# Optimization experiments

Measured on AMD Instinct MI355X. Metric: run time of the kernel, lower is better.

## Reference

```python
import jax, jax.numpy as jnp
import numpy as np

H, DK, DIM, DFF, DEPTH = 8, 64, 512, 2048, 8
B, LS, LT, VOCAB = 16, 128, 128, 32000


def setup_inputs() -> dict:
    key = jax.random.key(0)
    ks = jax.random.split(key, 20)
    w = lambda k, s: jax.random.normal(k, s, jnp.float32) * 0.02
    N_enc, N_dec = B * LS, B * LT
    base_s = np.arange(B) * LS
    base_t = np.arange(B) * LT
    i = np.arange(LS)
    j = np.arange(LT)
    # encoder self-attn: full bipartite within each sentence
    ee_src = (base_s[:, None, None] + i[None, :, None] + 0 * i[None, None, :]).reshape(-1)
    ee_dst = (base_s[:, None, None] + 0 * i[None, :, None] + i[None, None, :]).reshape(-1)
    # decoder self-attn: causal (key pos <= query pos)
    ii, jj = np.meshgrid(j, j, indexing='ij')  # ii = dst(query) pos, jj = src(key) pos
    m = jj <= ii
    dd_src = (base_t[:, None] + jj[m][None, :]).reshape(-1)
    dd_dst = (base_t[:, None] + ii[m][None, :]).reshape(-1)
    # cross-attn: enc node -> dec node, full within sentence
    ed_src = (base_s[:, None, None] + i[None, :, None] + 0 * j[None, None, :]).reshape(-1)
    ed_dst = (base_t[:, None, None] + 0 * i[None, :, None] + j[None, None, :]).reshape(-1)
    return {
        'emb_src': w(ks[0], (VOCAB, DIM)), 'emb_tgt': w(ks[1], (VOCAB, DIM)),
        'pos_emb': w(ks[2], (LS, DIM)), 'time_emb': w(ks[3], (DEPTH, DIM)),
        'Wqkv_e': w(ks[4], (DIM, 3 * DIM)), 'Wo_e': w(ks[5], (DIM, DIM)),
        'W1_e': w(ks[6], (DIM, DFF)), 'W2_e': w(ks[7], (DFF, DIM)),
        'Wqkv_d': w(ks[8], (DIM, 3 * DIM)), 'Wo_d': w(ks[9], (DIM, DIM)),
        'W1_d': w(ks[10], (DIM, DFF)), 'W2_d': w(ks[11], (DFF, DIM)),
        'Wq_x': w(ks[12], (DIM, DIM)), 'Wkv_x': w(ks[13], (DIM, 2 * DIM)),
        'Wo_x': w(ks[14], (DIM, DIM)), 'Wgen': w(ks[15], (DIM, VOCAB)),
        'src_tokens': jax.random.randint(ks[16], (N_enc,), 0, VOCAB, jnp.int32),
        'tgt_tokens': jax.random.randint(ks[17], (N_dec,), 0, VOCAB, jnp.int32),
        'src_pos': jnp.tile(jnp.arange(LS, dtype=jnp.int32), B),
        'tgt_pos': jnp.tile(jnp.arange(LT, dtype=jnp.int32), B),
        'ee_src': jnp.asarray(ee_src, jnp.int32), 'ee_dst': jnp.asarray(ee_dst, jnp.int32),
        'dd_src': jnp.asarray(dd_src, jnp.int32), 'dd_dst': jnp.asarray(dd_dst, jnp.int32),
        'ed_src': jnp.asarray(ed_src, jnp.int32), 'ed_dst': jnp.asarray(ed_dst, jnp.int32),
    }


def _ln(x):
    m = x.mean(-1, keepdims=True)
    v = ((x - m) ** 2).mean(-1, keepdims=True)
    return (x - m) * jax.lax.rsqrt(v + 1e-5)


def _attn(q, k, v, src, dst, n_dst):
    # q: [Nq,H,DK] (dst side), k/v: [Nk,H,DK] (src side); edge lists [E]
    # src_dot_dst -> scaled_exp -> scatter-sum (src_mul_edge + sum, copy_edge + sum), then wv/z
    s = jnp.exp(jnp.einsum('ehd,ehd->eh', k[src], q[dst]) / np.float32(np.sqrt(DK)))  # [E,H]
    wv = jax.ops.segment_sum(s[:, :, None] * v[src], dst, num_segments=n_dst)  # [Nq,H,DK]
    z = jax.ops.segment_sum(s, dst, num_segments=n_dst)  # [Nq,H]
    return (wv / (z[:, :, None] + 1e-9)).reshape(n_dst, DIM)


def reference(emb_src, emb_tgt, pos_emb, time_emb, Wqkv_e, Wo_e, W1_e, W2_e,
              Wqkv_d, Wo_d, W1_d, W2_d, Wq_x, Wkv_x, Wo_x, Wgen,
              src_tokens, tgt_tokens, src_pos, tgt_pos,
              ee_src, ee_dst, dd_src, dd_dst, ed_src, ed_dst):
    Ne, Nd = src_tokens.shape[0], tgt_tokens.shape[0]
    x_e = emb_src[src_tokens] + pos_emb[src_pos]
    x_d = emb_tgt[tgt_tokens] + pos_emb[tgt_pos]
    # encoder: MAX_DEPTH shared-weight iterations with time+pos enc re-added each step
    for t in range(DEPTH):
        xp = x_e + pos_emb[src_pos] + time_emb[t]
        q, k, v = jnp.split(xp @ Wqkv_e, 3, axis=-1)
        o = _attn(q.reshape(Ne, H, DK), k.reshape(Ne, H, DK), v.reshape(Ne, H, DK), ee_src, ee_dst, Ne)
        x_e = _ln(x_e + o @ Wo_e)
        x_e = _ln(x_e + jax.nn.relu(x_e @ W1_e) @ W2_e)
    # decoder: self-attn (causal dd) then cross-attn (ed) each iteration
    for t in range(DEPTH):
        xp = x_d + pos_emb[tgt_pos] + time_emb[t]
        q, k, v = jnp.split(xp @ Wqkv_d, 3, axis=-1)
        o = _attn(q.reshape(Nd, H, DK), k.reshape(Nd, H, DK), v.reshape(Nd, H, DK), dd_src, dd_dst, Nd)
        x_d = _ln(x_d + o @ Wo_d)
        qx = ((x_d + pos_emb[tgt_pos] + time_emb[t]) @ Wq_x).reshape(Nd, H, DK)
        kx, vx = jnp.split(x_e @ Wkv_x, 2, axis=-1)
        o = _attn(qx, kx.reshape(Ne, H, DK), vx.reshape(Ne, H, DK), ed_src, ed_dst, Nd)
        x_d = _ln(x_d + o @ Wo_x)
        x_d = _ln(x_d + jax.nn.relu(x_d @ W1_d) @ W2_d)
    return jax.nn.log_softmax(x_d @ Wgen, axis=-1)  # generator over dec nodes
```

## Files before the change

### kernel.cpp

```cpp
#include <hip/hip_runtime.h>
#include <hip/hip_bf16.h>
#include <math.h>

#define H 8
#define DK 64
#define DIM 512
#define DFF 2048
#define DEPTH 8
#define VOCAB 32000
#define NTOK 2048

typedef float f32x4 __attribute__((ext_vector_type(4)));
typedef short bf16x8 __attribute__((ext_vector_type(8)));

static __device__ __forceinline__ unsigned short f2bf(float f) {
    unsigned u = __float_as_uint(f);
    return (unsigned short)((u + 0x7FFFu + ((u >> 16) & 1u)) >> 16);
}

#define GLL(src, dst) __builtin_amdgcn_global_load_lds( \
    (const __attribute__((address_space(1))) unsigned int*)(src), \
    (__attribute__((address_space(3))) unsigned int*)(dst), 16, 0, 0)

static __device__ __forceinline__ void load_ln_stats(
// ... 79 lines not shown

    for (int k0 = 0; k0 < K; k0 += 64) {
        if (k0) __syncthreads();
#pragma unroll
        for (int it = 0; it < 4; it++) {
            int q = (wid * 4 + it) * 64 + lane;
            int row = q >> 3;
            int cs = (q & 7) ^ (row & 7);
            GLL(Bt + (size_t)(n0 + row) * K + k0 + cs * 8, &Bsm[(wid * 4 + it) * 512]);
        }
#pragma unroll
        for (int it = 0; it < 4; it++) {
            int q = (wid * 4 + it) * 64 + lane;
            int row = q >> 3;
            int cs = q & 7;
            const float* s = Tf + (size_t)(m0 + row) * K + k0 + cs * 8;
            float4 u0 = *(const float4*)s, u1 = *(const float4*)(s + 4);
            float m = Lm[row], iv = Li[row];
            unsigned short c8[8];
            c8[0] = f2bf((u0.x - m) * iv); c8[1] = f2bf((u0.y - m) * iv);
            c8[2] = f2bf((u0.z - m) * iv); c8[3] = f2bf((u0.w - m) * iv);
            c8[4] = f2bf((u1.x - m) * iv); c8[5] = f2bf((u1.y - m) * iv);
            c8[6] = f2bf((u1.z - m) * iv); c8[7] = f2bf((u1.w - m) * iv);
            *(bf16x8*)&Asm[row * 64 + ((cs ^ (row & 7)) * 8)] = *(bf16x8*)c8;
        }
        __syncthreads();
#pragma unroll
        for (int kk = 0; kk < 2; kk++) {
            bf16x8 af[4], bfr[4];
#pragma unroll
            for (int i = 0; i < 4; i++) {
                int rowA = wm + i * 16 + (lane & 15);
                int ca = (kk * 4 + (lane >> 4)) ^ (rowA & 7);
                af[i] = *(const bf16x8*)&Asm[rowA * 64 + ca * 8];
                int rowB = wn + i * 16 + (lane & 15);
                int cb = (kk * 4 + (lane >> 4)) ^ (rowB & 7);
                bfr[i] = *(const bf16x8*)&Bsm[rowB * 64 + cb * 8];
            }
#pragma unroll
            for (int i = 0; i < 4; i++)
#pragma unroll
                for (int j = 0; j < 4; j++)
                    acc[i][j] = __builtin_amdgcn_mfma_f32_16x16x32_bf16(af[i], bfr[j], acc[i][j], 0, 0, 0);
        }
    }
#pragma unroll
    for (int i = 0; i < 4; i++)
#pragma unroll
        for (int j = 0; j < 4; j++)
#pragma unroll
            for (int r = 0; r < 4; r++) {
                int row = m0 + wm + i * 16 + (lane >> 4) * 4 + r;
                int col = n0 + wn + j * 16 + (lane & 15);
                size_t idx = (size_t)row * N + col;
                float v = acc[i][j][r];
                if (EPI == 1) Cb[idx] = f2bf(fmaxf(v, 0.f));
                if (EPI == 3) Cb[idx] = f2bf(v);
            }
}

__global__ __launch_bounds__(256) void gemm_bb(
    const unsigned short* __restrict__ A,
    const unsigned short* __restrict__ Bt,
    const float* __restrict__ Tin,
    const float* __restrict__ statsIn,
    float* __restrict__ Tout,
    float* __restrict__ statsOut,
    int M, int K)
{
    __shared__ __align__(16) unsigned short Asm[64 * 64];
    __shared__ __align__(16) unsigned short Bsm[64 * 64];
    __shared__ float Lm[64], Li[64];
    __shared__ float sredS[4][64], sredQ[4][64];
    const int tid = threadIdx.x;
    const int lane = tid & 63, wid = tid >> 6;
    const int nb = blockIdx.x;
    const int m0 = blockIdx.y * 64, n0 = nb * 64;
    const int wm = (wid >> 1) * 32, wn = (wid & 1) * 32;

    load_ln_stats(statsIn, m0, 64, Lm, Li, tid, 256);
    __syncthreads();

    f32x4 acc[2][2];
#pragma unroll
    for (int i = 0; i < 2; i++)
#pragma unroll
        for (int j = 0; j < 2; j++) acc[i][j] = (f32x4){0.f, 0.f, 0.f, 0.f};

    for (int k0 = 0; k0 < K; k0 += 64) {
        if (k0) __syncthreads();
#pragma unroll
        for (int it = 0; it < 2; it++) {
            int q = it * 256 + tid;
            int row = q >> 3;
            int cs = (q & 7) ^ (row & 7);
            GLL(A + (size_t)(m0 + row) * K + k0 + cs * 8, &Asm[(it * 256 + wid * 64) * 8]);
            GLL(Bt + (size_t)(n0 + row) * K + k0 + cs * 8, &Bsm[(it * 256 + wid * 64) * 8]);
        }
        __syncthreads();
#pragma unroll
        for (int kd = 0; kd < 2; kd++) {
            bf16x8 af[2], bfr[2];
#pragma unroll
            for (int i = 0; i < 2; i++) {
                int rowA = wm + i * 16 + (lane & 15);
                int ca = (kd * 4 + (lane >> 4)) ^ (rowA & 7);
                af[i] = *(const bf16x8*)&Asm[rowA * 64 + ca * 8];
                int rowB = wn + i * 16 + (lane & 15);
                int cb = (kd * 4 + (lane >> 4)) ^ (rowB & 7);
                bfr[i] = *(const bf16x8*)&Bsm[rowB * 64 + cb * 8];
            }
#pragma unroll
            for (int i = 0; i < 2; i++)
#pragma unroll
                for (int j = 0; j < 2; j++)
                    acc[i][j] = __builtin_amdgcn_mfma_f32_16x16x32_bf16(af[i], bfr[j], acc[i][j], 0, 0, 0);
        }
    }
#pragma unroll
    for (int i = 0; i < 2; i++) {
#pragma unroll
        for (int r = 0; r < 4; r++) {
            int rl = wm + i * 16 + (lane >> 4) * 4 + r;
            int row = m0 + rl;
            float s = 0.f, q = 0.f;
#pragma unroll
            for (int j = 0; j < 2; j++) {
                int col = n0 + wn + j * 16 + (lane & 15);
                size_t idx = (size_t)row * DIM + col;
                float rv = (Tin[idx] - Lm[rl]) * Li[rl];
                float v = acc[i][j][r] + rv;
                Tout[idx] = v;
                s += v; q += v * v;
            }
            s += __shfl_xor(s, 1); s += __shfl_xor(s, 2);
            s += __shfl_xor(s, 4); s += __shfl_xor(s, 8);
            q += __shfl_xor(q, 1); q += __shfl_xor(q, 2);
            q += __shfl_xor(q, 4); q += __shfl_xor(q, 8);
            if ((lane & 15) == 0) { sredS[wid][rl] = s; sredQ[wid][rl] = q; }
        }
    }
    __syncthreads();
    if (tid < 64) {
        int row = tid;
        int w0 = (row >= 32) ? 2 : 0;
        float s = sredS[w0][row] + sredS[w0 + 1][row];
        float q = sredQ[w0][row] + sredQ[w0 + 1][row];
        statsOut[(size_t)(m0 + row) * 16 + nb * 2] = s;
        statsOut[(size_t)(m0 + row) * 16 + nb * 2 + 1] = q;
    }
}

template<int CAUSAL>
static __device__ __forceinline__ void attn_core16(
    const unsigned short* Qs, const unsigned short* Ks, const unsigned short* Vt,
    unsigned short* Psw, int wq, int lane, int tok0, int h,
    unsigned short* __restrict__ O)
{
    bf16x8 qa[2];
#pragma unroll
    for (int kd = 0; kd < 2; kd++) {
        int qr = wq + (lane & 15);
        int ch = (kd * 4 + (lane >> 4)) ^ (qr & 7);
        qa[kd] = *(const bf16x8*)&Qs[qr * 64 + ch * 8];
    }
    const int kcmax = CAUSAL ? ((wq >> 5) + 1) : 4;
    const int jmax = CAUSAL ? (kcmax * 2) : 8;

    float zr[4] = {0.f, 0.f, 0.f, 0.f};
    f32x4 oacc[4];
#pragma unroll
    for (int dt = 0; dt < 4; dt++) oacc[dt] = (f32x4){0.f, 0.f, 0.f, 0.f};

    for (int kb = 0; kb < 2; kb++) {
        int j0 = kb * 4;
        if (j0 >= jmax) break;
        int jn = jmax - j0; if (jn > 4) jn = 4;
        f32x4 sacc[4];
#pragma unroll
        for (int j = 0; j < 4; j++) sacc[j] = (f32x4){0.f, 0.f, 0.f, 0.f};
#pragma unroll 2
        for (int kd = 0; kd < 2; kd++) {
            for (int jj = 0; jj < jn; jj++) {
                int kr = (j0 + jj) * 16 + (lane & 15);
                int ch = (kd * 4 + (lane >> 4)) ^ (kr & 7);
                bf16x8 kf = *(const bf16x8*)&Ks[kr * 64 + ch * 8];
                sacc[jj] = __builtin_amdgcn_mfma_f32_16x16x32_bf16(qa[kd], kf, sacc[jj], 0, 0, 0);
            }
        }
        int qbase = wq + (lane >> 4) * 4;
        for (int jj = 0; jj < jn; jj++) {
            int kcol = (j0 + jj) * 16 + (lane & 15);
#pragma unroll
            for (int rr = 0; rr < 4; rr++) {
                float p = __expf(sacc[jj][rr] * 0.125f);
                if (CAUSAL && kcol > qbase + rr) p = 0.f;
                zr[rr] += p;
                int prow = (lane >> 4) * 4 + rr;
                int ch = ((jj * 2 + ((lane & 15) >> 3)) ^ (prow & 7));
                Psw[prow * 64 + ch * 8 + (lane & 7)] = f2bf(p);
            }
        }
        int kcn = kcmax - kb * 2; if (kcn > 2) kcn = 2;
        for (int kcl = 0; kcl < kcn; kcl++) {
            bf16x8 pa;
            {
                int prow = lane & 15;
                int ch = (kcl * 4 + (lane >> 4)) ^ (prow & 7);
                pa = *(const bf16x8*)&Psw[prow * 64 + ch * 8];
            }
            int kcg = kb * 2 + kcl;
#pragma unroll
            for (int dt = 0; dt < 4; dt++) {
                int d = dt * 16 + (lane & 15);
                bf16x8 vf = *(const bf16x8*)&Vt[d * 132 + (kcg * 4 + (lane >> 4)) * 8];
                oacc[dt] = __builtin_amdgcn_mfma_f32_16x16x32_bf16(pa, vf, oacc[dt], 0, 0, 0);
            }
        }
    }
#pragma unroll
    for (int rr = 0; rr < 4; rr++) {
        float z = zr[rr];
        z += __shfl_xor(z, 1); z += __shfl_xor(z, 2);
        z += __shfl_xor(z, 4); z += __shfl_xor(z, 8);
        zr[rr] = 1.f / (z + 1e-9f);
    }
#pragma unroll
    for (int dt = 0; dt < 4; dt++)
#pragma unroll
        for (int rr = 0; rr < 4; rr++) {
            int qrow = tok0 + wq + (lane >> 4) * 4 + rr;
            O[(size_t)qrow * DIM + h * 64 + dt * 16 + (lane & 15)] =
                f2bf(oacc[dt][rr] * zr[rr]);
        }
}

template<int CAUSAL>
__global__ __launch_bounds__(512) void fused_attn(
    const float* __restrict__ Tf,
    const float* __restrict__ stats,
    const float* __restrict__ pos,
    const float* __restrict__ trow,
    const unsigned short* __restrict__ WqkvT,
    unsigned short* __restrict__ O)
{
    __shared__ __align__(16) unsigned short smem[33024];
    __shared__ float LmA[128], LiA[128];
    unsigned short* Asm = smem;
    unsigned short* Bsm = smem + 8192;
    unsigned short* Qs  = smem;
    unsigned short* Ks  = smem + 8192;
    unsigned short* Vt  = smem + 16384;
    const int tid = threadIdx.x;
    const int lane = tid & 63, wid = tid >> 6;
    unsigned short* Psw = smem + 24832 + wid * 1024;
    const int b = blockIdx.x >> 3, h = blockIdx.x & 7;
    const int tok0 = b * 128;
    const int wq = wid * 16;

    load_ln_stats(stats, tok0, 128, LmA, LiA, tid, 512);
    __syncthreads();

    f32x4 acc[12];
#pragma unroll
    for (int c = 0; c < 12; c++) acc[c] = (f32x4){0.f, 0.f, 0.f, 0.f};

    for (int k0 = 0; k0 < 512; k0 += 64) {
        if (k0) __syncthreads();
#pragma unroll
        for (int it = 0; it < 3; it++) {
            int q = it * 512 + wid * 64 + lane;
            int r = q >> 3;
            int cs = (q & 7) ^ (r & 7);
            int srow = (r < 64) ? (h * 64 + r)
                     : (r < 128) ? (512 + h * 64 + (r - 64))
                                 : (1024 + h * 64 + (r - 128));
            GLL(WqkvT + (size_t)srow * 512 + k0 + cs * 8, &Bsm[(it * 512 + wid * 64) * 8]);
        }
#pragma unroll
        for (int it = 0; it < 2; it++) {
            int q = it * 512 + tid;
            int row = q >> 3;
            int cs = q & 7;
            const float* s = Tf + (size_t)(tok0 + row) * 512 + k0 + cs * 8;
            const float* pp = pos + (size_t)row * 512 + k0 + cs * 8;
            const float* tt = trow + k0 + cs * 8;
            float4 u0 = *(const float4*)s, u1 = *(const float4*)(s + 4);
            float4 p0 = *(const float4*)pp, p1 = *(const float4*)(pp + 4);
            float4 t0 = *(const float4*)tt, t1 = *(const float4*)(tt + 4);
            float m = LmA[row], iv = LiA[row];
            unsigned short c8[8];
            c8[0] = f2bf((u0.x - m) * iv + p0.x + t0.x);
            c8[1] = f2bf((u0.y - m) * iv + p0.y + t0.y);
            c8[2] = f2bf((u0.z - m) * iv + p0.z + t0.z);
            c8[3] = f2bf((u0.w - m) * iv + p0.w + t0.w);
            c8[4] = f2bf((u1.x - m) * iv + p1.x + t1.x);
            c8[5] = f2bf((u1.y - m) * iv + p1.y + t1.y);
            c8[6] = f2bf((u1.z - m) * iv + p1.z + t1.z);
            c8[7] = f2bf((u1.w - m) * iv + p1.w + t1.w);
            *(bf16x8*)&Asm[row * 64 + ((cs ^ (row & 7)) * 8)] = *(bf16x8*)c8;
        }
        __syncthreads();
#pragma unroll
        for (int kk = 0; kk < 2; kk++) {
            int rowA = wq + (lane & 15);
            int ca = (kk * 4 + (lane >> 4)) ^ (rowA & 7);
            bf16x8 af = *(const bf16x8*)&Asm[rowA * 64 + ca * 8];
#pragma unroll
            for (int c = 0; c < 12; c++) {
                int rowB = c * 16 + (lane & 15);
                int cb = (kk * 4 + (lane >> 4)) ^ (rowB & 7);
                bf16x8 bfr = *(const bf16x8*)&Bsm[rowB * 64 + cb * 8];
                acc[c] = __builtin_amdgcn_mfma_f32_16x16x32_bf16(af, bfr, acc[c], 0, 0, 0);
            }
        }
    }
    __syncthreads();
#pragma unroll
    for (int c = 0; c < 12; c++)
#pragma unroll
        for (int r = 0; r < 4; r++) {
            int token = wq + (lane >> 4) * 4 + r;
            int col = (c & 3) * 16 + (lane & 15);
            unsigned short v = f2bf(acc[c][r]);
            if (c < 4)      Qs[token * 64 + (((col >> 3) ^ (token & 7)) * 8) + (col & 7)] = v;
            else if (c < 8) Ks[token * 64 + (((col >> 3) ^ (token & 7)) * 8) + (col & 7)] = v;
            else            Vt[col * 132 + token] = v;
        }
    __syncthreads();
    attn_core16<CAUSAL>(Qs, Ks, Vt, Psw, wq, lane, tok0, h, O);
}

__global__ __launch_bounds__(512) void fused_xattn(
    const float* __restrict__ Tf,
    const float* __restrict__ stats,
    const float* __restrict__ pos,
    const float* __restrict__ trow,
    const unsigned short* __restrict__ WqT,
    const unsigned short* __restrict__ kvx,
    unsigned short* __restrict__ O)
{
    __shared__ __align__(16) unsigned short smem[33024];
    __shared__ float LmA[128], LiA[128];
    unsigned short* Asm = smem;
    unsigned short* Bsm = smem + 8192;
    unsigned short* Qs  = smem;
    unsigned short* Ks  = smem + 8192;
    unsigned short* Vt  = smem + 16384;
    const int tid = threadIdx.x;
    const int lane = tid & 63, wid = tid >> 6;
    unsigned short* Psw = smem + 24832 + wid * 1024;
    const int b = blockIdx.x >> 3, h = blockIdx.x & 7;
    const int tok0 = b * 128;
    const int wq = wid * 16;

    load_ln_stats(stats, tok0, 128, LmA, LiA, tid, 512);
    __syncthreads();

    f32x4 acc[4];
#pragma unroll
    for (int c = 0; c < 4; c++) acc[c] = (f32x4){0.f, 0.f, 0.f, 0.f};

    for (int k0 = 0; k0 < 512; k0 += 64) {
        if (k0) __syncthreads();
        {
            int q = wid * 64 + lane;
            int r = q >> 3;
            int cs = (q & 7) ^ (r & 7);
            GLL(WqT + (size_t)(h * 64 + r) * 512 + k0 + cs * 8, &Bsm[(wid * 64) * 8]);
        }
#pragma unroll
        for (int it = 0; it < 2; it++) {
            int q = it * 512 + tid;
            int row = q >> 3;
            int cs = q & 7;
            const float* s = Tf + (size_t)(tok0 + row) * 512 + k0 + cs * 8;
            const float* pp = pos + (size_t)row * 512 + k0 + cs * 8;
            const float* tt = trow + k0 + cs * 8;
            float4 u0 = *(const float4*)s, u1 = *(const float4*)(s + 4);
            float4 p0 = *(const float4*)pp, p1 = *(const float4*)(pp + 4);
            float4 t0 = *(const float4*)tt, t1 = *(const float4*)(tt + 4);
            float m = LmA[row], iv = LiA[row];
            unsigned short c8[8];
            c8[0] = f2bf((u0.x - m) * iv + p0.x + t0.x);
            c8[1] = f2bf((u0.y - m) * iv + p0.y + t0.y);
            c8[2] = f2bf((u0.z - m) * iv + p0.z + t0.z);
            c8[3] = f2bf((u0.w - m) * iv + p0.w + t0.w);
            c8[4] = f2bf((u1.x - m) * iv + p1.x + t1.x);
            c8[5] = f2bf((u1.y - m) * iv + p1.y + t1.y);
            c8[6] = f2bf((u1.z - m) * iv + p1.z + t1.z);
            c8[7] = f2bf((u1.w - m) * iv + p1.w + t1.w);
            *(bf16x8*)&Asm[row * 64 + ((cs ^ (row & 7)) * 8)] = *(bf16x8*)c8;
        }
        __syncthreads();
#pragma unroll
        for (int kk = 0; kk < 2; kk++) {
            int rowA = wq + (lane & 15);
            int ca = (kk * 4 + (lane >> 4)) ^ (rowA & 7);
            bf16x8 af = *(const bf16x8*)&Asm[rowA * 64 + ca * 8];
#pragma unroll
            for (int c = 0; c < 4; c++) {
                int rowB = c * 16 + (lane & 15);
                int cb = (kk * 4 + (lane >> 4)) ^ (rowB & 7);
                bf16x8 bfr = *(const bf16x8*)&Bsm[rowB * 64 + cb * 8];
                acc[c] = __builtin_amdgcn_mfma_f32_16x16x32_bf16(af, bfr, acc[c], 0, 0, 0);
            }
        }
    }
    __syncthreads();
#pragma unroll
    for (int c = 0; c < 4; c++)
#pragma unroll
        for (int r = 0; r < 4; r++) {
            int token = wq + (lane >> 4) * 4 + r;
            int col = c * 16 + (lane & 15);
            Qs[token * 64 + (((col >> 3) ^ (token & 7)) * 8) + (col & 7)] = f2bf(acc[c][r]);
        }
    {
        int r = tid >> 2, c0 = (tid & 3) * 2;
        const unsigned short* Kg = kvx + (size_t)(tok0 + r) * 1024 + h * 64;
        const unsigned short* Vg = Kg + 512;
#pragma unroll
        for (int c = c0; c < c0 + 2; c++) {
            bf16x8 kv = *(const bf16x8*)&Kg[c * 8];
            *(bf16x8*)&Ks[r * 64 + ((c ^ (r & 7)) * 8)] = kv;
            bf16x8 vv = *(const bf16x8*)&Vg[c * 8];
#pragma unroll
            for (int j = 0; j < 8; j++)
                Vt[(c * 8 + j) * 132 + r] = (unsigned short)vv[j];
        }
    }
    __syncthreads();
    attn_core16<0>(Qs, Ks, Vt, Psw, wq, lane, tok0, h, O);
}

__global__ __launch_bounds__(64) void ln_fin(const float* __restrict__ T,
                                             const float* __restrict__ stats,
                                             unsigned short* __restrict__ outb) {
    const int row = blockIdx.x, lane = threadIdx.x;
    const float* st = stats + (size_t)row * 16;
    float sum = 0.f, sq = 0.f;
#pragma unroll
    for (int b = 0; b < 8; b++) { sum += st[b * 2]; sq += st[b * 2 + 1]; }
    float m = sum * (1.f / 512.f);
    float v = sq * (1.f / 512.f) - m * m;
    float inv = 1.f / sqrtf(v + 1e-5f);
    const float* p = T + (size_t)row * DIM;
    unsigned short* qb = outb + (size_t)row * DIM;
#pragma unroll
    for (int i = 0; i < 8; i++)
        qb[lane + i * 64] = f2bf((p[lane + i * 64] - m) * inv);
}

__global__ __launch_bounds__(512) void gemm_gen(
    const unsigned short* __restrict__ Ab,
    const unsigned short* __restrict__ Bt,
    float* __restrict__ Out,
    float* __restrict__ pm,
    float* __restrict__ psum)
{
    __shared__ __align__(16) unsigned short Asm[256 * 64];
    __shared__ __align__(16) unsigned short Bsm[128 * 64];
    __shared__ float pml[8][64];
    __shared__ float psl[8][64];
    const int tid = threadIdx.x;
    const int lane = tid & 63, wid = tid >> 6;
    const int m0 = blockIdx.x * 256, n0 = blockIdx.y * 128;
    const int wm = (wid >> 1) * 64, wn = (wid & 1) * 64;

    f32x4 acc[4][4];
#pragma unroll
    for (int i = 0; i < 4; i++)
#pragma unroll
        for (int j = 0; j < 4; j++) acc[i][j] = (f32x4){0.f, 0.f, 0.f, 0.f};

    for (int k0 = 0; k0 < 512; k0 += 64) {
        if (k0) __syncthreads();
#pragma unroll
        for (int it = 0; it < 2; it++) {
            int q = it * 512 + tid;
            int row = q >> 3;
            int cs = (q & 7) ^ (row & 7);
            GLL(Bt + (size_t)(n0 + row) * 512 + k0 + cs * 8, &Bsm[(it * 512 + wid * 64) * 8]);
        }
#pragma unroll
        for (int it = 0; it < 4; it++) {
            int q = it * 512 + tid;
            int row = q >> 3;
            int cs = (q & 7) ^ (row & 7);
            GLL(Ab + (size_t)(m0 + row) * 512 + k0 + cs * 8, &Asm[(it * 512 + wid * 64) * 8]);
        }
        __syncthreads();
#pragma unroll
        for (int kk = 0; kk < 2; kk++) {
            bf16x8 af[4], bfr[4];
#pragma unroll
            for (int i = 0; i < 4; i++) {
                int rowA = wm + i * 16 + (lane & 15);
                int ca = (kk * 4 + (lane >> 4)) ^ (rowA & 7);
                af[i] = *(const bf16x8*)&Asm[rowA * 64 + ca * 8];
                int rowB = wn + i * 16 + (lane & 15);
                int cb = (kk * 4 + (lane >> 4)) ^ (rowB & 7);
                bfr[i] = *(const bf16x8*)&Bsm[rowB * 64 + cb * 8];
            }
#pragma unroll
            for (int i = 0; i < 4; i++)
#pragma unroll
                for (int j = 0; j < 4; j++)
                    acc[i][j] = __builtin_amdgcn_mfma_f32_16x16x32_bf16(af[i], bfr[j], acc[i][j], 0, 0, 0);
        }
    }
#pragma unroll
    for (int i = 0; i < 4; i++) {
#pragma unroll
        for (int r = 0; r < 4; r++) {
            float mx = fmaxf(fmaxf(acc[i][0][r], acc[i][1][r]),
                             fmaxf(acc[i][2][r], acc[i][3][r]));
            mx = fmaxf(mx, __shfl_xor(mx, 1));
            mx = fmaxf(mx, __shfl_xor(mx, 2));
            mx = fmaxf(mx, __shfl_xor(mx, 4));
            mx = fmaxf(mx, __shfl_xor(mx, 8));
            float s = __expf(acc[i][0][r] - mx) + __expf(acc[i][1][r] - mx) +
                      __expf(acc[i][2][r] - mx) + __expf(acc[i][3][r] - mx);
            s += __shfl_xor(s, 1); s += __shfl_xor(s, 2);
            s += __shfl_xor(s, 4); s += __shfl_xor(s, 8);
            if ((lane & 15) == 0) {
                int li = i * 16 + (lane >> 4) * 4 + r;
                pml[wid][li] = mx;
                psl[wid][li] = s;
            }
        }
    }
    __syncthreads();
    if (tid < 256) {
        int g = tid >> 6, lr = tid & 63;
        int wa = g * 2, wb = g * 2 + 1;
        float ma = pml[wa][lr], mb = pml[wb][lr];
        float m = fmaxf(ma, mb);
        float s = psl[wa][lr] * __expf(ma - m) + psl[wb][lr] * __expf(mb - m);
        pm[(size_t)(m0 + g * 64 + lr) * 256 + blockIdx.y] = m;
        psum[(size_t)(m0 + g * 64 + lr) * 256 + blockIdx.y] = s;
    }
#pragma unroll
    for (int i = 0; i < 4; i++)
#pragma unroll
        for (int j = 0; j < 4; j++)
#pragma unroll
            for (int r = 0; r < 4; r++) {
                int row = m0 + wm + i * 16 + (lane >> 4) * 4 + r;
                int col = n0 + wn + j * 16 + (lane & 15);
                Out[(size_t)row * VOCAB + col] = acc[i][j][r];
            }
}

__global__ __launch_bounds__(256) void sub_kernel(float* __restrict__ out,
                                                  const float* __restrict__ pm,
                                                  const float* __restrict__ psum) {
    const int row = blockIdx.x, tid = threadIdx.x;
    const int lane = tid & 63, wid = tid >> 6;
    __shared__ float ms[4], ss[4];
    float m = -1e30f, s = 0.f;
    for (int nb = tid; nb < 250; nb += 256) {
        float mm = pm[(size_t)row * 256 + nb];
        float sv = psum[(size_t)row * 256 + nb];
        float M = fmaxf(m, mm);
        s = s * __expf(m - M) + sv * __expf(mm - M);
        m = M;
    }
#pragma unroll
    for (int off = 32; off > 0; off >>= 1) {
        float mo = __shfl_xor(m, off), so = __shfl_xor(s, off);
        float M = fmaxf(m, mo);
        s = s * __expf(m - M) + so * __expf(mo - M);
        m = M;
    }
    if (lane == 0) { ms[wid] = m; ss[wid] = s; }
    __syncthreads();
    float M = fmaxf(fmaxf(ms[0], ms[1]), fmaxf(ms[2], ms[3]));
    float S = ss[0] * __expf(ms[0] - M) + ss[1] * __expf(ms[1] - M) +
              ss[2] * __expf(ms[2] - M) + ss[3] * __expf(ms[3] - M);
    const float lse = M + __logf(S);
    float4* p = (float4*)(out + (size_t)row * VOCAB);
    for (int i = tid; i < VOCAB / 4; i += 256) {
        float4 v = p[i];
        p[i] = make_float4(v.x - lse, v.y - lse, v.z - lse, v.w - lse);
    }
}

extern "C" void kernel_launch(void* const* d_in, const int* in_sizes, int n_in,
                              void* d_out, int out_size, void* d_ws, size_t ws_size,
                              hipStream_t stream) {
    const float* emb_src  = (const float*)d_in[0];
    const float* emb_tgt  = (const float*)d_in[1];
    const float* pos_emb  = (const float*)d_in[2];
    const float* time_emb = (const float*)d_in[3];
    const float* Wqkv_e   = (const float*)d_in[4];
    const float* Wo_e     = (const float*)d_in[5];
    const float* W1_e     = (const float*)d_in[6];
    const float* W2_e     = (const float*)d_in[7];
    const float* Wqkv_d   = (const float*)d_in[8];
    const float* Wo_d     = (const float*)d_in[9];
    const float* W1_d     = (const float*)d_in[10];
    const float* W2_d     = (const float*)d_in[11];
    const float* Wq_x     = (const float*)d_in[12];
    const float* Wkv_x    = (const float*)d_in[13];
    const float* Wo_x     = (const float*)d_in[14];
    const float* Wgen     = (const float*)d_in[15];
    const int* src_tokens = (const int*)d_in[16];
    const int* tgt_tokens = (const int*)d_in[17];
    const int* src_pos    = (const int*)d_in[18];
    const int* tgt_pos    = (const int*)d_in[19];

    char* w = (char*)d_ws;
    float* T_e0 = (float*)(w);
    float* T_e1 = (float*)(w + (4u << 20));
    float* T_d0 = (float*)(w + (8u << 20));
    float* T_d1 = (float*)(w + (12u << 20));
    float* T_d2 = (float*)(w + (16u << 20));
    unsigned short* kvx_bf = (unsigned short*)(w + (20u << 20));
    unsigned short* o_bf   = (unsigned short*)(w + (24u << 20));
    unsigned short* hid_bf = (unsigned short*)(w + (26u << 20));
    unsigned short* xd_bf  = (unsigned short*)(w + (34u << 20));
    float* pm   = (float*)(w + (36u << 20));
    float* psum = (float*)(w + (38u << 20));
    float* se0  = (float*)(w + (40u << 20));
    float* se1  = se0 + 32768;
    float* sd0  = se1 + 32768;
    float* sd1  = sd0 + 32768;
    float* sd2  = sd1 + 32768;
    unsigned short* wts = (unsigned short*)(w + (41u << 20));

    unsigned short* WqkvE_t = wts;
    unsigned short* WoE_t   = WqkvE_t + 786432;
    unsigned short* W1E_t   = WoE_t   + 262144;
    unsigned short* W2E_t   = W1E_t   + 1048576;
    unsigned short* WqkvD_t = W2E_t   + 1048576;
    unsigned short* WoD_t   = WqkvD_t + 786432;
    unsigned short* W1D_t   = WoD_t   + 262144;
    unsigned short* W2D_t   = W1D_t   + 1048576;
    unsigned short* WqX_t   = W2D_t   + 1048576;
    unsigned short* WkvX_t  = WqX_t   + 262144;
    unsigned short* WoX_t   = WkvX_t  + 524288;
    unsigned short* Wgen_t  = WoX_t   + 262144;

    float* out = (float*)d_out;

    WTab tab;
    auto set = [&](int i, const float* s, unsigned short* d, int K, int N, int t0) {
        tab.d[i].src = s; tab.d[i].dst = d; tab.d[i].K = K; tab.d[i].N = N;
        tab.d[i].t0 = t0; tab.d[i].pad = 0;
    };
    set(0,  Wqkv_e, WqkvE_t, 512, 1536, 0);
    set(1,  Wo_e,   WoE_t,   512, 512,  768);
    set(2,  W1_e,   W1E_t,   512, 2048, 1024);
    set(3,  W2_e,   W2E_t,   2048, 512, 2048);
    set(4,  Wqkv_d, WqkvD_t, 512, 1536, 3072);
    set(5,  Wo_d,   WoD_t,   512, 512,  3840);
    set(6,  W1_d,   W1D_t,   512, 2048, 4096);
    set(7,  W2_d,   W2D_t,   2048, 512, 5120);
    set(8,  Wq_x,   WqX_t,   512, 512,  6144);
    set(9,  Wkv_x,  WkvX_t,  512, 1024, 6400);
    set(10, Wo_x,   WoX_t,   512, 512,  6912);
    set(11, Wgen,   Wgen_t,  512, 32000, 7168);
    wconv_all<<<23168, 256, 0, stream>>>(tab);

    const int n4 = NTOK * (DIM / 4);
    dim3 eb(256), eg((n4 + 255) / 256);
    embed_kernel<<<eg, eb, 0, stream>>>(emb_src, src_tokens, pos_emb, src_pos, T_e0, n4);
    embed_kernel<<<eg, eb, 0, stream>>>(emb_tgt, tgt_tokens, pos_emb, tgt_pos, T_d0, n4);

    const dim3 gFF(DFF / 128, NTOK / 128), gKV(1024 / 128, NTOK / 128),
               gBB(8, NTOK / 64);

    {
        const float* scur = nullptr;
        for (int t = 0; t < DEPTH; t++) {
            const float* trow = time_emb + (size_t)t * DIM;
            fused_attn<0><<<128, 512, 0, stream>>>(T_e0, scur, pos_emb, trow, WqkvE_t, o_bf);
            gemm_bb<<<gBB, 256, 0, stream>>>(o_bf, WoE_t, T_e0, scur, T_e1, se0, NTOK, 512);
            gemm_rb<1><<<gFF, 256, 0, stream>>>(T_e1, se0, W1E_t, hid_bf, NTOK, DFF, 512);
            gemm_bb<<<gBB, 256, 0, stream>>>(hid_bf, W2E_t, T_e1, se0, T_e0, se1, NTOK, 2048);
            scur = se1;
        }
    }

    gemm_rb<3><<<gKV, 256, 0, stream>>>(T_e0, se1, WkvX_t, kvx_bf, NTOK, 1024, 512);

    {
        const float* scur = nullptr;
        for (int t = 0; t < DEPTH; t++) {
            const float* trow = time_emb + (size_t)t * DIM;
            fused_attn<1><<<128, 512, 0, stream>>>(T_d0, scur, pos_emb, trow, WqkvD_t, o_bf);
            gemm_bb<<<gBB, 256, 0, stream>>>(o_bf, WoD_t, T_d0, scur, T_d1, sd0, NTOK, 512);

            fused_xattn<<<128, 512, 0, stream>>>(T_d1, sd0, pos_emb, trow, WqX_t, kvx_bf, o_bf);
            gemm_bb<<<gBB, 256, 0, stream>>>(o_bf, WoX_t, T_d1, sd0, T_d2, sd1, NTOK, 512);

            gemm_rb<1><<<gFF, 256, 0, stream>>>(T_d2, sd1, W1D_t, hid_bf, NTOK, DFF, 512);
            gemm_bb<<<gBB, 256, 0, stream>>>(hid_bf, W2D_t, T_d2, sd1, T_d0, sd2, NTOK, 2048);
            scur = sd2;
        }
    }

    ln_fin<<<NTOK, 64, 0, stream>>>(T_d0, sd2, xd_bf);
    gemm_gen<<<dim3(8, 250), 512, 0, stream>>>(xd_bf, Wgen_t, out, pm, psum);
    sub_kernel<<<NTOK, 256, 0, stream>>>(out, pm, psum);
}
```

Measured before the change: 1.857 ms.

## Split attention blocks by query half and recompute generator logits for log-softmax

```diff
diff --git a/kernel.cpp b/kernel.cpp
--- a/kernel.cpp
+++ b/kernel.cpp
@@ -255,45 +255,47 @@
 }
 
 template<int CAUSAL>
-static __device__ __forceinline__ void attn_core16(
+static __device__ __forceinline__ void attn_phase2_split(
     const unsigned short* Qs, const unsigned short* Ks, const unsigned short* Vt,
-    unsigned short* Psw, int wq, int lane, int tok0, int h,
+    unsigned short* Psw, float* dumpf,
+    int qh, int wid, int lane, int tok0, int h,
     unsigned short* __restrict__ O)
 {
+    const int qg = wid & 3, kh = wid >> 2;
     bf16x8 qa[2];
 #pragma unroll
     for (int kd = 0; kd < 2; kd++) {
-        int qr = wq + (lane & 15);
+        int qr = qg * 16 + (lane & 15);
         int ch = (kd * 4 + (lane >> 4)) ^ (qr & 7);
         qa[kd] = *(const bf16x8*)&Qs[qr * 64 + ch * 8];
     }
-    const int kcmax = CAUSAL ? ((wq >> 5) + 1) : 4;
-    const int jmax = CAUSAL ? (kcmax * 2) : 8;
+    int jn, kcn;
+    if (!CAUSAL)      { jn = 4; kcn = 2; }
+    else if (kh > qh) { jn = 0; kcn = 0; }
+    else if (kh < qh) { jn = 4; kcn = 2; }
+    else              { kcn = (qg >> 1) + 1; jn = kcn * 2; }
 
     float zr[4] = {0.f, 0.f, 0.f, 0.f};
     f32x4 oacc[4];
 #pragma unroll
     for (int dt = 0; dt < 4; dt++) oacc[dt] = (f32x4){0.f, 0.f, 0.f, 0.f};
 
-    for (int kb = 0; kb < 2; kb++) {
-        int j0 = kb * 4;
-        if (j0 >= jmax) break;
-        int jn = jmax - j0; if (jn > 4) jn = 4;
+    if (jn > 0) {
         f32x4 sacc[4];
 #pragma unroll
         for (int j = 0; j < 4; j++) sacc[j] = (f32x4){0.f, 0.f, 0.f, 0.f};
 #pragma unroll 2
         for (int kd = 0; kd < 2; kd++) {
             for (int jj = 0; jj < jn; jj++) {
-                int kr = (j0 + jj) * 16 + (lane & 15);
+                int kr = kh * 64 + jj * 16 + (lane & 15);
                 int ch = (kd * 4 + (lane >> 4)) ^ (kr & 7);
                 bf16x8 kf = *(const bf16x8*)&Ks[kr * 64 + ch * 8];
                 sacc[jj] = __builtin_amdgcn_mfma_f32_16x16x32_bf16(qa[kd], kf, sacc[jj], 0, 0, 0);
             }
         }
-        int qbase = wq + (lane >> 4) * 4;
+        int qbase = qh * 64 + qg * 16 + (lane >> 4) * 4;
         for (int jj = 0; jj < jn; jj++) {
-            int kcol = (j0 + jj) * 16 + (lane & 15);
+            int kcol = kh * 64 + jj * 16 + (lane & 15);
 #pragma unroll
             for (int rr = 0; rr < 4; rr++) {
                 float p = __expf(sacc[jj][rr] * 0.125f);
@@ -304,7 +306,6 @@
                 Psw[prow * 64 + ch * 8 + (lane & 7)] = f2bf(p);
             }
         }
-        int kcn = kcmax - kb * 2; if (kcn > 2) kcn = 2;
         for (int kcl = 0; kcl < kcn; kcl++) {
             bf16x8 pa;
             {
@@ -312,7 +313,7 @@
                 int ch = (kcl * 4 + (lane >> 4)) ^ (prow & 7);
                 pa = *(const bf16x8*)&Psw[prow * 64 + ch * 8];
             }
-            int kcg = kb * 2 + kcl;
+            int kcg = kh * 2 + kcl;
 #pragma unroll
             for (int dt = 0; dt < 4; dt++) {
                 int d = dt * 16 + (lane & 15);
@@ -321,21 +322,39 @@
             }
         }
     }
-#pragma unroll
-    for (int rr = 0; rr < 4; rr++) {
-        float z = zr[rr];
-        z += __shfl_xor(z, 1); z += __shfl_xor(z, 2);
-        z += __shfl_xor(z, 4); z += __shfl_xor(z, 8);
-        zr[rr] = 1.f / (z + 1e-9f);
-    }
-#pragma unroll
-    for (int dt = 0; dt < 4; dt++)
+    __syncthreads();
+    if (kh == 1) {
+        float* dst = dumpf + (size_t)(qg * 64 + lane) * 20;
+#pragma unroll
+        for (int dt = 0; dt < 4; dt++)
+#pragma unroll
+            for (int rr = 0; rr < 4; rr++) dst[dt * 4 + rr] = oacc[dt][rr];
+#pragma unroll
+        for (int rr = 0; rr < 4; rr++) dst[16 + rr] = zr[rr];
+    }
+    __syncthreads();
+    if (kh == 0) {
+        const float* src = dumpf + (size_t)(qg * 64 + lane) * 20;
+#pragma unroll
+        for (int dt = 0; dt < 4; dt++)
+#pragma unroll
+            for (int rr = 0; rr < 4; rr++) oacc[dt][rr] += src[dt * 4 + rr];
 #pragma unroll
         for (int rr = 0; rr < 4; rr++) {
-            int qrow = tok0 + wq + (lane >> 4) * 4 + rr;
-            O[(size_t)qrow * DIM + h * 64 + dt * 16 + (lane & 15)] =
-                f2bf(oacc[dt][rr] * zr[rr]);
-        }
+            float z = zr[rr] + src[16 + rr];
+            z += __shfl_xor(z, 1); z += __shfl_xor(z, 2);
+            z += __shfl_xor(z, 4); z += __shfl_xor(z, 8);
+            zr[rr] = 1.f / (z + 1e-9f);
+        }
+#pragma unroll
+        for (int dt = 0; dt < 4; dt++)
+#pragma unroll
+            for (int rr = 0; rr < 4; rr++) {
+                int qrow = tok0 + qh * 64 + qg * 16 + (lane >> 4) * 4 + rr;
+                O[(size_t)qrow * DIM + h * 64 + dt * 16 + (lane & 15)] =
+                    f2bf(oacc[dt][rr] * zr[rr]);
+            }
+    }
 }
 
 template<int CAUSAL>
@@ -347,19 +366,21 @@
     const unsigned short* __restrict__ WqkvT,
     unsigned short* __restrict__ O)
 {
-    __shared__ __align__(16) unsigned short smem[33024];
+    __shared__ __align__(16) unsigned short smem[28928];
     __shared__ float LmA[128], LiA[128];
     unsigned short* Asm = smem;
     unsigned short* Bsm = smem + 8192;
     unsigned short* Qs  = smem;
-    unsigned short* Ks  = smem + 8192;
-    unsigned short* Vt  = smem + 16384;
+    unsigned short* Ks  = smem + 4096;
+    unsigned short* Vt  = smem + 12288;
+    float* dumpf = (float*)smem;
     const int tid = threadIdx.x;
     const int lane = tid & 63, wid = tid >> 6;
-    unsigned short* Psw = smem + 24832 + wid * 1024;
-    const int b = blockIdx.x >> 3, h = blockIdx.x & 7;
+    unsigned short* Psw = smem + 20736 + wid * 1024;
+    const int blk = blockIdx.x;
+    const int qh = blk & 1, h = (blk >> 1) & 7, b = blk >> 4;
     const int tok0 = b * 128;
-    const int wq = wid * 16;
+    const int wr = wid * 16;
 
     load_ln_stats(stats, tok0, 128, LmA, LiA, tid, 512);
     __syncthreads();
@@ -406,7 +427,7 @@
         __syncthreads();
 #pragma unroll
         for (int kk = 0; kk < 2; kk++) {
-            int rowA = wq + (lane & 15);
+            int rowA = wr + (lane & 15);
             int ca = (kk * 4 + (lane >> 4)) ^ (rowA & 7);
             bf16x8 af = *(const bf16x8*)&Asm[rowA * 64 + ca * 8];
 #pragma unroll
@@ -423,15 +444,21 @@
     for (int c = 0; c < 12; c++)
 #pragma unroll
         for (int r = 0; r < 4; r++) {
-            int token = wq + (lane >> 4) * 4 + r;
+            int token = wr + (lane >> 4) * 4 + r;
             int col = (c & 3) * 16 + (lane & 15);
             unsigned short v = f2bf(acc[c][r]);
-            if (c < 4)      Qs[token * 64 + (((col >> 3) ^ (token & 7)) * 8) + (col & 7)] = v;
-            else if (c < 8) Ks[token * 64 + (((col >> 3) ^ (token & 7)) * 8) + (col & 7)] = v;
-            else            Vt[col * 132 + token] = v;
-        }
-    __syncthreads();
-    attn_core16<CAUSAL>(Qs, Ks, Vt, Psw, wq, lane, tok0, h, O);
+            if (c < 4) {
+                int tl = token - qh * 64;
+                if (tl >= 0 && tl < 64)
+                    Qs[tl * 64 + (((col >> 3) ^ (tl & 7)) * 8) + (col & 7)] = v;
+            } else if (c < 8) {
+                Ks[token * 64 + (((col >> 3) ^ (token & 7)) * 8) + (col & 7)] = v;
+            } else {
+                Vt[col * 132 + token] = v;
+            }
+        }
+    __syncthreads();
+    attn_phase2_split<CAUSAL>(Qs, Ks, Vt, Psw, dumpf, qh, wid, lane, tok0, h, O);
 }
 
 __global__ __launch_bounds__(512) void fused_xattn(
@@ -443,88 +470,30 @@
     const unsigned short* __restrict__ kvx,
     unsigned short* __restrict__ O)
 {
-    __shared__ __align__(16) unsigned short smem[33024];
-    __shared__ float LmA[128], LiA[128];
-    unsigned short* Asm = smem;
-    unsigned short* Bsm = smem + 8192;
+    __shared__ __align__(16) unsigned short smem[28928];
+    __shared__ float LmA[64], LiA[64];
     unsigned short* Qs  = smem;
-    unsigned short* Ks  = smem + 8192;
-    unsigned short* Vt  = smem + 16384;
+    unsigned short* Ks  = smem + 4096;
+    unsigned short* Vt  = smem + 12288;
+    unsigned short* Asm = smem + 20736;
+    unsigned short* Bsm = smem + 24832;
+    float* dumpf = (float*)smem;
     const int tid = threadIdx.x;
     const int lane = tid & 63, wid = tid >> 6;
-    unsigned short* Psw = smem + 24832 + wid * 1024;
-    const int b = blockIdx.x >> 3, h = blockIdx.x & 7;
+    unsigned short* Psw = smem + 20736 + wid * 1024;
+    const int blk = blockIdx.x;
+    const int qh = blk & 1, h = (blk >> 1) & 7, b = blk >> 4;
     const int tok0 = b * 128;
-    const int wq = wid * 16;
-
-    load_ln_stats(stats, tok0, 128, LmA, LiA, tid, 512);
-    __syncthreads();
-
-    f32x4 acc[4];
-#pragma unroll
-    for (int c = 0; c < 4; c++) acc[c] = (f32x4){0.f, 0.f, 0.f, 0.f};
-
-    for (int k0 = 0; k0 < 512; k0 += 64) {
-        if (k0) __syncthreads();
-        {
-            int q = wid * 64 + lane;
-            int r = q >> 3;
-            int cs = (q & 7) ^ (r & 7);
-            GLL(WqT + (size_t)(h * 64 + r) * 512 + k0 + cs * 8, &Bsm[(wid * 64) * 8]);
-        }
-#pragma unroll
-        for (int it = 0; it < 2; it++) {
-            int q = it * 512 + tid;
-            int row = q >> 3;
-            int cs = q & 7;
-            const float* s = Tf + (size_t)(tok0 + row) * 512 + k0 + cs * 8;
-            const float* pp = pos + (size_t)row * 512 + k0 + cs * 8;
-            const float* tt = trow + k0 + cs * 8;
-            float4 u0 = *(const float4*)s, u1 = *(const float4*)(s + 4);
-            float4 p0 = *(const float4*)pp, p1 = *(const float4*)(pp + 4);
-            float4 t0 = *(const float4*)tt, t1 = *(const float4*)(tt + 4);
-            float m = LmA[row], iv = LiA[row];
-            unsigned short c8[8];
-            c8[0] = f2bf((u0.x - m) * iv + p0.x + t0.x);
-            c8[1] = f2bf((u0.y - m) * iv + p0.y + t0.y);
-            c8[2] = f2bf((u0.z - m) * iv + p0.z + t0.z);
-            c8[3] = f2bf((u0.w - m) * iv + p0.w + t0.w);
-            c8[4] = f2bf((u1.x - m) * iv + p1.x + t1.x);
-            c8[5] = f2bf((u1.y - m) * iv + p1.y + t1.y);
-            c8[6] = f2bf((u1.z - m) * iv + p1.z + t1.z);
-            c8[7] = f2bf((u1.w - m) * iv + p1.w + t1.w);
-            *(bf16x8*)&Asm[row * 64 + ((cs ^ (row & 7)) * 8)] = *(bf16x8*)c8;
-        }
-        __syncthreads();
-#pragma unroll
-        for (int kk = 0; kk < 2; kk++) {
-            int rowA = wq + (lane & 15);
-            int ca = (kk * 4 + (lane >> 4)) ^ (rowA & 7);
-            bf16x8 af = *(const bf16x8*)&Asm[rowA * 64 + ca * 8];
-#pragma unroll
-            for (int c = 0; c < 4; c++) {
-                int rowB = c * 16 + (lane & 15);
-                int cb = (kk * 4 + (lane >> 4)) ^ (rowB & 7);
-                bf16x8 bfr = *(const bf16x8*)&Bsm[rowB * 64 + cb * 8];
-                acc[c] = __builtin_amdgcn_mfma_f32_16x16x32_bf16(af, bfr, acc[c], 0, 0, 0);
-            }
-        }
-    }
-    __syncthreads();
-#pragma unroll
-    for (int c = 0; c < 4; c++)
-#pragma unroll
-        for (int r = 0; r < 4; r++) {
-            int token = wq + (lane >> 4) * 4 + r;
-            int col = c * 16 + (lane & 15);
-            Qs[token * 64 + (((col >> 3) ^ (token & 7)) * 8) + (col & 7)] = f2bf(acc[c][r]);
-        }
-    {
-        int r = tid >> 2, c0 = (tid & 3) * 2;
+
+    load_ln_stats(stats, tok0 + qh * 64, 64, LmA, LiA, tid, 512);
+
+    if (wid >= 4) {
+        int st = tid - 256;
+        int r = st >> 1, c0 = (st & 1) * 4;
         const unsigned short* Kg = kvx + (size_t)(tok0 + r) * 1024 + h * 64;
         const unsigned short* Vg = Kg + 512;
 #pragma unroll
-        for (int c = c0; c < c0 + 2; c++) {
+        for (int c = c0; c < c0 + 4; c++) {
             bf16x8 kv = *(const bf16x8*)&Kg[c * 8];
             *(bf16x8*)&Ks[r * 64 + ((c ^ (r & 7)) * 8)] = kv;
             bf16x8 vv = *(const bf16x8*)&Vg[c * 8];
@@ -534,7 +503,75 @@
         }
     }
     __syncthreads();
-    attn_core16<0>(Qs, Ks, Vt, Psw, wq, lane, tok0, h, O);
+
+    f32x4 acc[4];
+#pragma unroll
+    for (int c = 0; c < 4; c++) acc[c] = (f32x4){0.f, 0.f, 0.f, 0.f};
+
+    for (int k0 = 0; k0 < 512; k0 += 64) {
+        if (k0) __syncthreads();
+        if (tid < 256) {
+#pragma unroll
+            for (int it = 0; it < 2; it++) {
+                int q = it * 256 + tid;
+                int r = q >> 3;
+                int cs = (q & 7) ^ (r & 7);
+                GLL(WqT + (size_t)(h * 64 + r) * 512 + k0 + cs * 8, &Bsm[((q >> 3) * 8 + ((q & 7) * 0)) * 0 + (it * 256 + (tid >> 0)) * 0 + q * 0 + (it * 256 + tid) * 8]);
+            }
+#pragma unroll
+            for (int it = 0; it < 2; it++) {
+                int q = it * 256 + tid;
+                int row = q >> 3;
+                int cs = q & 7;
+                const float* s = Tf + (size_t)(tok0 + qh * 64 + row) * 512 + k0 + cs * 8;
+                const float* pp = pos + (size_t)(qh * 64 + row) * 512 + k0 + cs * 8;
+                const float* tt = trow + k0 + cs * 8;
+                float4 u0 = *(const float4*)s, u1 = *(const float4*)(s + 4);
+                float4 p0 = *(const float4*)pp, p1 = *(const float4*)(pp + 4);
+                float4 t0 = *(const float4*)tt, t1 = *(const float4*)(tt + 4);
+                float m = LmA[row], iv = LiA[row];
+                unsigned short c8[8];
+                c8[0] = f2bf((u0.x - m) * iv + p0.x + t0.x);
+                c8[1] = f2bf((u0.y - m) * iv + p0.y + t0.y);
+                c8[2] = f2bf((u0.z - m) * iv + p0.z + t0.z);
+                c8[3] = f2bf((u0.w - m) * iv + p0.w + t0.w);
+                c8[4] = f2bf((u1.x - m) * iv + p1.x + t1.x);
+                c8[5] = f2bf((u1.y - m) * iv + p1.y + t1.y);
+                c8[6] = f2bf((u1.z - m) * iv + p1.z + t1.z);
+                c8[7] = f2bf((u1.w - m) * iv + p1.w + t1.w);
+                *(bf16x8*)&Asm[row * 64 + ((cs ^ (row & 7)) * 8)] = *(bf16x8*)c8;
+            }
+        }
+        __syncthreads();
+        if (wid < 4) {
+#pragma unroll
+            for (int kk = 0; kk < 2; kk++) {
+                int rowA = wid * 16 + (lane & 15);
+                int ca = (kk * 4 + (lane >> 4)) ^ (rowA & 7);
+                bf16x8 af = *(const bf16x8*)&Asm[rowA * 64 + ca * 8];
+#pragma unroll
+                for (int c = 0; c < 4; c++) {
+                    int rowB = c * 16 + (lane & 15);
+                    int cb = (kk * 4 + (lane >> 4)) ^ (rowB & 7);
+                    bf16x8 bfr = *(const bf16x8*)&Bsm[rowB * 64 + cb * 8];
+                    acc[c] = __builtin_amdgcn_mfma_f32_16x16x32_bf16(af, bfr, acc[c], 0, 0, 0);
+                }
+            }
+        }
+    }
+    __syncthreads();
+    if (wid < 4) {
+#pragma unroll
+        for (int c = 0; c < 4; c++)
+#pragma unroll
+            for (int r = 0; r < 4; r++) {
+                int tl = wid * 16 + (lane >> 4) * 4 + r;
+                int col = c * 16 + (lane & 15);
+                Qs[tl * 64 + (((col >> 3) ^ (tl & 7)) * 8) + (col & 7)] = f2bf(acc[c][r]);
+            }
+    }
+    __syncthreads();
+    attn_phase2_split<0>(Qs, Ks, Vt, Psw, dumpf, qh, wid, lane, tok0, h, O);
 }
 
 __global__ __launch_bounds__(64) void ln_fin(const float* __restrict__ T,
@@ -555,22 +592,33 @@
         qb[lane + i * 64] = f2bf((p[lane + i * 64] - m) * inv);
 }
 
+template<int PASS>
 __global__ __launch_bounds__(512) void gemm_gen(
     const unsigned short* __restrict__ Ab,
     const unsigned short* __restrict__ Bt,
     float* __restrict__ Out,
     float* __restrict__ pm,
-    float* __restrict__ psum)
+    float* __restrict__ psum,
+    const float* __restrict__ lse)
 {
     __shared__ __align__(16) unsigned short Asm[256 * 64];
     __shared__ __align__(16) unsigned short Bsm[128 * 64];
     __shared__ float pml[8][64];
     __shared__ float psl[8][64];
+    __shared__ float lsh[256];
     const int tid = threadIdx.x;
     const int lane = tid & 63, wid = tid >> 6;
-    const int m0 = blockIdx.x * 256, n0 = blockIdx.y * 128;
+    const int d = blockIdx.x + blockIdx.y * 8;
+    const int t = (d & 7) * 250 + (d >> 3);
+    const int mt = t & 7, nt = t >> 3;
+    const int m0 = mt * 256, n0 = nt * 128;
     const int wm = (wid >> 1) * 64, wn = (wid & 1) * 64;
 
+    if (PASS == 1) {
+        for (int r = tid; r < 256; r += 512) lsh[r] = lse[m0 + r];
+        __syncthreads();
+    }
+
     f32x4 acc[4][4];
 #pragma unroll
     for (int i = 0; i < 4; i++)
@@ -578,7 +626,7 @@
         for (int j = 0; j < 4; j++) acc[i][j] = (f32x4){0.f, 0.f, 0.f, 0.f};
 
     for (int k0 = 0; k0 < 512; k0 += 64) {
-        if (k0) __syncthreads();
+        if (k0 || PASS == 1) __syncthreads();
 #pragma unroll
         for (int it = 0; it < 2; it++) {
             int q = it * 512 + tid;
@@ -613,61 +661,61 @@
                     acc[i][j] = __builtin_amdgcn_mfma_f32_16x16x32_bf16(af[i], bfr[j], acc[i][j], 0, 0, 0);
         }
     }
-#pragma unroll
-    for (int i = 0; i < 4; i++) {
-#pragma unroll
-        for (int r = 0; r < 4; r++) {
-            float mx = fmaxf(fmaxf(acc[i][0][r], acc[i][1][r]),
-                             fmaxf(acc[i][2][r], acc[i][3][r]));
-            mx = fmaxf(mx, __shfl_xor(mx, 1));
-            mx = fmaxf(mx, __shfl_xor(mx, 2));
-            mx = fmaxf(mx, __shfl_xor(mx, 4));
-            mx = fmaxf(mx, __shfl_xor(mx, 8));
-            float s = __expf(acc[i][0][r] - mx) + __expf(acc[i][1][r] - mx) +
-                      __expf(acc[i][2][r] - mx) + __expf(acc[i][3][r] - mx);
-            s += __shfl_xor(s, 1); s += __shfl_xor(s, 2);
-            s += __shfl_xor(s, 4); s += __shfl_xor(s, 8);
-            if ((lane & 15) == 0) {
-                int li = i * 16 + (lane >> 4) * 4 + r;
-                pml[wid][li] = mx;
-                psl[wid][li] = s;
-            }
-        }
-    }
-    __syncthreads();
-    if (tid < 256) {
-        int g = tid >> 6, lr = tid & 63;
-        int wa = g * 2, wb = g * 2 + 1;
-        float ma = pml[wa][lr], mb = pml[wb][lr];
-        float m = fmaxf(ma, mb);
-        float s = psl[wa][lr] * __expf(ma - m) + psl[wb][lr] * __expf(mb - m);
-        pm[(size_t)(m0 + g * 64 + lr) * 256 + blockIdx.y] = m;
-        psum[(size_t)(m0 + g * 64 + lr) * 256 + blockIdx.y] = s;
-    }
-#pragma unroll
-    for (int i = 0; i < 4; i++)
-#pragma unroll
-        for (int j = 0; j < 4; j++)
+    if (PASS == 0) {
+#pragma unroll
+        for (int i = 0; i < 4; i++) {
 #pragma unroll
             for (int r = 0; r < 4; r++) {
-                int row = m0 + wm + i * 16 + (lane >> 4) * 4 + r;
-                int col = n0 + wn + j * 16 + (lane & 15);
-                Out[(size_t)row * VOCAB + col] = acc[i][j][r];
-            }
-}
-
-__global__ __launch_bounds__(256) void sub_kernel(float* __restrict__ out,
-                                                  const float* __restrict__ pm,
-                                                  const float* __restrict__ psum) {
-    const int row = blockIdx.x, tid = threadIdx.x;
-    const int lane = tid & 63, wid = tid >> 6;
-    __shared__ float ms[4], ss[4];
+                float mx = fmaxf(fmaxf(acc[i][0][r], acc[i][1][r]),
+                                 fmaxf(acc[i][2][r], acc[i][3][r]));
+                mx = fmaxf(mx, __shfl_xor(mx, 1));
+                mx = fmaxf(mx, __shfl_xor(mx, 2));
+                mx = fmaxf(mx, __shfl_xor(mx, 4));
+                mx = fmaxf(mx, __shfl_xor(mx, 8));
+                float s = __expf(acc[i][0][r] - mx) + __expf(acc[i][1][r] - mx) +
+                          __expf(acc[i][2][r] - mx) + __expf(acc[i][3][r] - mx);
+                s += __shfl_xor(s, 1); s += __shfl_xor(s, 2);
+                s += __shfl_xor(s, 4); s += __shfl_xor(s, 8);
+                if ((lane & 15) == 0) {
+                    int li = i * 16 + (lane >> 4) * 4 + r;
+                    pml[wid][li] = mx;
+                    psl[wid][li] = s;
+                }
+            }
+        }
+        __syncthreads();
+        if (tid < 256) {
+            int g = tid >> 6, lr = tid & 63;
+            int wa = g * 2, wb = g * 2 + 1;
+            float m = fmaxf(pml[wa][lr], pml[wb][lr]);
+            float s = psl[wa][lr] * __expf(pml[wa][lr] - m) + psl[wb][lr] * __expf(pml[wb][lr] - m);
+            pm[(size_t)(m0 + g * 64 + lr) * 256 + nt] = m;
+            psum[(size_t)(m0 + g * 64 + lr) * 256 + nt] = s;
+        }
+    } else {
+#pragma unroll
+        for (int i = 0; i < 4; i++)
+#pragma unroll
+            for (int j = 0; j < 4; j++)
+#pragma unroll
+                for (int r = 0; r < 4; r++) {
+                    int rl = wm + i * 16 + (lane >> 4) * 4 + r;
+                    int col = n0 + wn + j * 16 + (lane & 15);
+                    Out[(size_t)(m0 + rl) * VOCAB + col] = acc[i][j][r] - lsh[rl];
+                }
+    }
+}
+
+__global__ __launch_bounds__(64) void lse_kernel(const float* __restrict__ pm,
+                                                 const float* __restrict__ psum,
+                                                 float* __restrict__ lse) {
+    const int row = blockIdx.x, t = threadIdx.x;
     float m = -1e30f, s = 0.f;
-    for (int nb = tid; nb < 250; nb += 256) {
+    for (int nb = t; nb < 250; nb += 64) {
         float mm = pm[(size_t)row * 256 + nb];
-        float sv = psum[(size_t)row * 256 + nb];
+        float ss = psum[(size_t)row * 256 + nb];
         float M = fmaxf(m, mm);
-        s = s * __expf(m - M) + sv * __expf(mm - M);
+        s = s * __expf(m - M) + ss * __expf(mm - M);
         m = M;
     }
 #pragma unroll
@@ -677,17 +725,7 @@
         s = s * __expf(m - M) + so * __expf(mo - M);
         m = M;
     }
-    if (lane == 0) { ms[wid] = m; ss[wid] = s; }
-    __syncthreads();
-    float M = fmaxf(fmaxf(ms[0], ms[1]), fmaxf(ms[2], ms[3]));
-    float S = ss[0] * __expf(ms[0] - M) + ss[1] * __expf(ms[1] - M) +
-              ss[2] * __expf(ms[2] - M) + ss[3] * __expf(ms[3] - M);
-    const float lse = M + __logf(S);
-    float4* p = (float4*)(out + (size_t)row * VOCAB);
-    for (int i = tid; i < VOCAB / 4; i += 256) {
-        float4 v = p[i];
-        p[i] = make_float4(v.x - lse, v.y - lse, v.z - lse, v.w - lse);
-    }
+    if (t == 0) lse[row] = m + __logf(s);
 }
 
 extern "C" void kernel_launch(void* const* d_in, const int* in_sizes, int n_in,
@@ -731,6 +769,7 @@
     float* sd0  = se1 + 32768;
     float* sd1  = sd0 + 32768;
     float* sd2  = sd1 + 32768;
+    float* lse  = sd2 + 32768;
     unsigned short* wts = (unsigned short*)(w + (41u << 20));
 
     unsigned short* WqkvE_t = wts;
@@ -779,7 +818,7 @@
         const float* scur = nullptr;
         for (int t = 0; t < DEPTH; t++) {
             const float* trow = time_emb + (size_t)t * DIM;
-            fused_attn<0><<<128, 512, 0, stream>>>(T_e0, scur, pos_emb, trow, WqkvE_t, o_bf);
+            fused_attn<0><<<256, 512, 0, stream>>>(T_e0, scur, pos_emb, trow, WqkvE_t, o_bf);
             gemm_bb<<<gBB, 256, 0, stream>>>(o_bf, WoE_t, T_e0, scur, T_e1, se0, NTOK, 512);
             gemm_rb<1><<<gFF, 256, 0, stream>>>(T_e1, se0, W1E_t, hid_bf, NTOK, DFF, 512);
             gemm_bb<<<gBB, 256, 0, stream>>>(hid_bf, W2E_t, T_e1, se0, T_e0, se1, NTOK, 2048);
@@ -793,10 +832,10 @@
         const float* scur = nullptr;
         for (int t = 0; t < DEPTH; t++) {
             const float* trow = time_emb + (size_t)t * DIM;
-            fused_attn<1><<<128, 512, 0, stream>>>(T_d0, scur, pos_emb, trow, WqkvD_t, o_bf);
+            fused_attn<1><<<256, 512, 0, stream>>>(T_d0, scur, pos_emb, trow, WqkvD_t, o_bf);
             gemm_bb<<<gBB, 256, 0, stream>>>(o_bf, WoD_t, T_d0, scur, T_d1, sd0, NTOK, 512);
 
-            fused_xattn<<<128, 512, 0, stream>>>(T_d1, sd0, pos_emb, trow, WqX_t, kvx_bf, o_bf);
+            fused_xattn<<<256, 512, 0, stream>>>(T_d1, sd0, pos_emb, trow, WqX_t, kvx_bf, o_bf);
             gemm_bb<<<gBB, 256, 0, stream>>>(o_bf, WoX_t, T_d1, sd0, T_d2, sd1, NTOK, 512);
 
             gemm_rb<1><<<gFF, 256, 0, stream>>>(T_d2, sd1, W1D_t, hid_bf, NTOK, DFF, 512);
@@ -806,6 +845,7 @@
     }
 
     ln_fin<<<NTOK, 64, 0, stream>>>(T_d0, sd2, xd_bf);
-    gemm_gen<<<dim3(8, 250), 512, 0, stream>>>(xd_bf, Wgen_t, out, pm, psum);
-    sub_kernel<<<NTOK, 256, 0, stream>>>(out, pm, psum);
-}
+    gemm_gen<0><<<dim3(8, 250), 512, 0, stream>>>(xd_bf, Wgen_t, nullptr, pm, psum, nullptr);
+    lse_kernel<<<NTOK, 64, 0, stream>>>(pm, psum, lse);
+    gemm_gen<1><<<dim3(8, 250), 512, 0, stream>>>(xd_bf, Wgen_t, out, nullptr, nullptr, lse);
+}
```

Result: faster. 1.750 ms (-5.8%).
